# Optimization experiments

Measured on AMD Instinct MI355X. Metric: run time of the kernel, lower is better.

## Reference

```python
import math
import jax, jax.numpy as jnp
import numpy as np


def setup_inputs() -> dict:
    key = jax.random.key(0)
    k0, k1, k2 = jax.random.split(key, 3)
    b, c, h, w = 4, 256, 64, 64
    x = jax.random.normal(k0, (b, c, h, w), dtype=jnp.float32)
    # 1x1 conv weights stored as [out_ch, in_ch]
    qkv_w = jax.random.normal(k1, (3 * c, c), dtype=jnp.float32) / math.sqrt(c)
    qkv_b = jnp.zeros((3 * c,), dtype=jnp.float32)
    out_w = jax.random.normal(k2, (c, c), dtype=jnp.float32) / math.sqrt(c)
    out_b = jnp.zeros((c,), dtype=jnp.float32)
    return {"x": x, "qkv_w": qkv_w, "qkv_b": qkv_b, "out_w": out_w, "out_b": out_b}


def reference(x, qkv_w, qkv_b, out_w, out_b):
    b, c, h, w = x.shape
    n = h * w
    # 1x1 conv QKV projection: [b, 3c, h, w]
    qkv = jnp.einsum('oc,bchw->bohw', qkv_w, x) + qkv_b[None, :, None, None]
    # chunk along channels into q, k, v each [b, c, n]
    qkv = qkv.reshape(b, 3, c, n)
    q, k, v = qkv[:, 0], qkv[:, 1], qkv[:, 2]
    # attn[b, i, j] = sum_c k[b,c,i] * q[b,c,j] / sqrt(c); softmax over key axis (dim=-2 -> axis=1)
    scores = jnp.einsum('bcn,bcm->bnm', k, q) / math.sqrt(c)
    attn = jax.nn.softmax(scores, axis=1)
    # out[b, c, j] = sum_i v[b,c,i] * attn[b,i,j]
    o = jnp.einsum('bcn,bnm->bcm', v, attn).reshape(b, c, h, w)
    # output 1x1 conv
    return jnp.einsum('oc,bchw->bohw', out_w, o) + out_b[None, :, None, None]
```

## Files before the change

### kernel.cpp

```cpp
#include <hip/hip_runtime.h>
#include <hip/hip_bf16.h>

typedef unsigned short u16;
typedef unsigned int u32;
typedef __attribute__((ext_vector_type(8))) short short8;
typedef __attribute__((ext_vector_type(4))) short short4v;
typedef __attribute__((ext_vector_type(16))) float f32x16;

#define MFMA32 __builtin_amdgcn_mfma_f32_32x32x16_bf16

#define NSEQ 4096
#define CD 256
#define CF 0.09016844005556021f

__device__ __forceinline__ u16 f2bf(float f) {
  u32 u = __float_as_uint(f);
  u += 0x7fffu + ((u >> 16) & 1u);
  return (u16)(u >> 16);
}
__device__ __forceinline__ float bf2f(short s) {
  return __uint_as_float(((u32)(u16)s) << 16);
}
__device__ __forceinline__ u32 pk2bf(float a, float b) {
  union {
    __hip_bfloat162 h;
    u32 u;
  } cv;
  cv.h = __float22bfloat162_rn(make_float2(a, b));
  return cv.u;
}
__device__ __forceinline__ void async16(const void* g, void* l) {
  __builtin_amdgcn_global_load_lds(
      (const __attribute__((address_space(1))) u32*)g,
      (__attribute__((address_space(3))) u32*)l, 16, 0, 0);
}

__global__ void cast_w(const float* __restrict__ qkv_w,
                       const float* __restrict__ out_w, u16* __restrict__ wq,
                       u16* __restrict__ wo) {
  int idx = blockIdx.x * 256 + threadIdx.x;
  if (idx < 768 * CD) wq[idx] = f2bf(qkv_w[idx]);
  if (idx < CD * CD) wo[idx] = f2bf(out_w[idx]);
}

__global__ __launch_bounds__(256) void xpose(const float* __restrict__ x,
                                             u16* __restrict__ x_t) {
  __shared__ float tile[64][65];
  const int t = threadIdx.x;
  const int b = blockIdx.z;
  const int n0 = blockIdx.x * 64, c0 = blockIdx.y * 64;
  const float* xb = x + (size_t)b * CD * NSEQ;
  const int cr = t >> 4, nc4 = (t & 15) * 4;
#pragma unroll
  for (int i = 0; i < 4; ++i) {
    int c = cr + 16 * i;
    float4 v = *(const float4*)(xb + (size_t)(c0 + c) * NSEQ + n0 + nc4);
    tile[c][nc4 + 0] = v.x;
    tile[c][nc4 + 1] = v.y;
    tile[c][nc4 + 2] = v.z;
    tile[c][nc4 + 3] = v.w;
  }
  __syncthreads();
  const int n = t & 63, cc = (t >> 6) * 16;
  u16* dst = x_t + (size_t)b * NSEQ * CD + (size_t)(n0 + n) * CD + c0 + cc;
#pragma unroll
  for (int j = 0; j < 4; ++j) {
    short4v pv;
#pragma unroll
    for (int r = 0; r < 4; ++r) pv[r] = (short)f2bf(tile[cc + 4 * j + r][n]);
    *(short4v*)(dst + 4 * j) = pv;
  }
}

__global__ __launch_bounds__(512, 1) void qkv_gemm3(
    const u16* __restrict__ wq, const float* __restrict__ qkv_b,
    const u16* __restrict__ x_t, u16* __restrict__ q_t, u16* __restrict__ k_t,
    u16* __restrict__ v_) {
  __shared__ u16 __align__(16) Wls[128 * 256];
  __shared__ u16 __align__(16) Bls[128 * 256];
  const int t = threadIdx.x, w = t >> 6, lane = t & 63;
  const int l31 = lane & 31, l5 = lane >> 5;
  const int os = w & 3, nh = w >> 2;
  const int n0 = blockIdx.x * 128, o0 = blockIdx.y * 128, b = blockIdx.z;
  const u16* Xb = x_t + (size_t)b * NSEQ * CD;
#pragma unroll
  for (int j = 0; j < 8; ++j) {
    int r = w * 16 + j * 2 + l5;
    async16(wq + (size_t)(o0 + r) * CD + ((l31 ^ (r & 7)) * 8),
            Wls + (w * 16 + j * 2) * 256);
    async16(Xb + (size_t)(n0 + r) * CD + ((l31 ^ (r & 7)) * 8),
            Bls + (w * 16 + j * 2) * 256);
  }
  __builtin_amdgcn_s_waitcnt(0);
  __syncthreads();
  f32x16 acc0, acc1;
#pragma unroll
  for (int i = 0; i < 16; ++i) {
    acc0[i] = 0.f;
    acc1[i] = 0.f;
  }
  const int ra = os * 32 + l31;
  const int rb0 = nh * 64 + l31, rb1 = rb0 + 32;
#pragma unroll
  for (int kc = 0; kc < 16; ++kc) {
    short8 a = *(const short8*)(Wls + ra * 256 + (((kc * 2 + l5) ^ (ra & 7)) * 8));
    short8 b0 = *(const short8*)(Bls + rb0 * 256 + (((kc * 2 + l5) ^ (rb0 & 7)) * 8));
    short8 b1 = *(const short8*)(Bls + rb1 * 256 + (((kc * 2 + l5) ^ (rb1 & 7)) * 8));
    acc0 = MFMA32(a, b0, acc0, 0, 0, 0);
    acc1 = MFMA32(a, b1, acc1, 0, 0, 0);
  }
  const int otype = blockIdx.y >> 1;
  const int obase = o0 + os * 32;
#pragma unroll
  for (int na = 0; na < 2; ++na) {
    f32x16& acc = na ? acc1 : acc0;
    const int n_g = n0 + nh * 64 + na * 32 + l31;
    if (otype < 2) {
      u16* dst = (otype == 0 ? q_t : k_t) + (size_t)b * NSEQ * CD +
                 (size_t)n_g * CD + (obase - otype * 256);
#pragma unroll
      for (int g = 0; g < 4; ++g) {
        float4 bv = *(const float4*)(qkv_b + obase + g * 8 + l5 * 4);
        const float* bp = (const float*)&bv;
        short4v pk;
#pragma unroll
        for (int r = 0; r < 4; ++r) pk[r] = (short)f2bf(acc[g * 4 + r] + bp[r]);
        *(short4v*)(dst + g * 8 + l5 * 4) = pk;
      }
    } else {
      u16* dst = v_ + (size_t)b * CD * NSEQ;
#pragma unroll
      for (int g = 0; g < 4; ++g) {
        float4 bv = *(const float4*)(qkv_b + obase + g * 8 + l5 * 4);
        const float* bp = (const float*)&bv;
#pragma unroll
        for (int r = 0; r < 4; ++r) {
          int c = obase - 512 + g * 8 + l5 * 4 + r;
          dst[(size_t)c * NSEQ + n_g] = f2bf(acc[g * 4 + r] + bp[r]);
        }
      }
    }
  }
}

__global__ __launch_bounds__(512, 1) void flash6(const u16* __restrict__ q_t,
                                                 const u16* __restrict__ k_t,
                                                 const u16* __restrict__ v_,
                                                 u16* __restrict__ opart,
                                                 float2* __restrict__ ml) {
  __shared__ u16 __align__(16) Kls[2][64 * 256];
  __shared__ u16 __align__(16) Vls[2][256 * 64];

  const int t = threadIdx.x, w = t >> 6, lane = t & 63;
  const int l31 = lane & 31, l5 = lane >> 5;
  const int s = w >> 1, ch = (w & 1) * 128;

  const int linear = blockIdx.x;
  const int xcd = linear & 7, slot = linear >> 3;
  const int b = xcd >> 1, half = xcd & 1;
  const int m0 = slot * 128;
  const int nbase = half * 2048;

  const u16* Qb = q_t + (size_t)b * NSEQ * CD;
  const u16* Kb = k_t + (size_t)b * NSEQ * CD;
  const u16* Vb = v_ + (size_t)b * CD * NSEQ;

  const int lm = s * 32 + l31;
  const int mrow = m0 + lm;

  short8 qf[16];
#pragma unroll
  for (int kc = 0; kc < 16; ++kc)
    qf[kc] = *(const short8*)(Qb + (size_t)mrow * CD + kc * 16 + l5 * 8);

  const int kr = w * 8;
  const int vrb = w * 32;
  const int vr_lane = lane >> 3, vc_lane = lane & 7;

#pragma unroll
  for (int j = 0; j < 4; ++j) {
    int r = kr + j * 2 + l5;
    async16(Kb + (size_t)(nbase + r) * CD + ((l31 ^ (r & 7)) * 8),
            &Kls[0][(kr + j * 2) * 256]);
    int rv = vrb + j * 8 + vr_lane;
    async16(Vb + (size_t)rv * NSEQ + nbase + ((vc_lane ^ (rv & 7)) * 8),
            &Vls[0][(vrb + j * 8) * 64]);
  }

  float mst = -3.0e38f, lst = 0.f;
  f32x16 oa[4];
#pragma unroll
  for (int i = 0; i < 4; ++i)
#pragma unroll
    for (int r = 0; r < 16; ++r) oa[i][r] = 0.f;

  for (int tt = 0; tt < 32; ++tt) {
    const int cur = tt & 1;
    __builtin_amdgcn_s_waitcnt(0);
    __syncthreads();
    if (tt + 1 < 32) {
      const int n0 = nbase + (tt + 1) * 64;
      const int nxt = cur ^ 1;
#pragma unroll
      for (int j = 0; j < 4; ++j) {
        int r = kr + j * 2 + l5;
        async16(Kb + (size_t)(n0 + r) * CD + ((l31 ^ (r & 7)) * 8),
                &Kls[nxt][(kr + j * 2) * 256]);
        int rv = vrb + j * 8 + vr_lane;
        async16(Vb + (size_t)rv * NSEQ + n0 + ((vc_lane ^ (rv & 7)) * 8),
                &Vls[nxt][(vrb + j * 8) * 64]);
      }
    }
    f32x16 sa, sb;
#pragma unroll
    for (int i = 0; i < 16; ++i) {
      sa[i] = 0.f;
      sb[i] = 0.f;
    }
    const int rk0 = l31, rk1 = 32 + l31;
#pragma unroll
    for (int kc = 0; kc < 16; ++kc) {
      short8 a0 =
          *(const short8*)(&Kls[cur][rk0 * 256 + (((kc * 2 + l5) ^ (l31 & 7)) * 8)]);
      short8 a1 =
          *(const short8*)(&Kls[cur][rk1 * 256 + (((kc * 2 + l5) ^ (l31 & 7)) * 8)]);
      sa = MFMA32(a0, qf[kc], sa, 0, 0, 0);
      sb = MFMA32(a1, qf[kc], sb, 0, 0, 0);
    }
    float rm = sa[0];
#pragma unroll
    for (int i = 1; i < 16; ++i) rm = fmaxf(rm, sa[i]);
#pragma unroll
    for (int i = 0; i < 16; ++i) rm = fmaxf(rm, sb[i]);
    rm = fmaxf(rm, __shfl_xor(rm, 32));
    float mnew = fmaxf(mst, rm * CF);
    float al = exp2f(mst - mnew);
    mst = mnew;
    u32 d[2][4][2];
    float ls = 0.f;
#pragma unroll
    for (int a = 0; a < 2; ++a) {
      f32x16& sv = a ? sb : sa;
#pragma unroll
      for (int gg = 0; gg < 4; ++gg) {
        float p0 = exp2f(sv[gg * 4 + 0] * CF - mnew);
        float p1 = exp2f(sv[gg * 4 + 1] * CF - mnew);
        float p2 = exp2f(sv[gg * 4 + 2] * CF - mnew);
        float p3 = exp2f(sv[gg * 4 + 3] * CF - mnew);
        ls += (p0 + p1) + (p2 + p3);
        d[a][gg][0] = pk2bf(p0, p1);
        d[a][gg][1] = pk2bf(p2, p3);
      }
    }
    ls += __shfl_xor(ls, 32);
    lst = lst * al + ls;
    if (__ballot(al != 1.0f)) {
#pragma unroll
      for (int i = 0; i < 4; ++i)
#pragma unroll
        for (int r = 0; r < 16; ++r) oa[i][r] *= al;
    }
    short8 pf[4];
#pragma unroll
    for (int f = 0; f < 4; ++f) {
      const int a = f >> 1, g0 = (f & 1) * 2;
      u32 n0d = d[a][g0][0], n1d = d[a][g0][1];
      u32 m0d = d[a][g0 + 1][0], m1d = d[a][g0 + 1][1];
      u32 s0 = l5 ? n0d : m0d;
      u32 s1 = l5 ? n1d : m1d;
      u32 e0 = (u32)__shfl_xor((int)s0, 32);
      u32 e1 = (u32)__shfl_xor((int)s1, 32);
      union {
        u32 u[4];
        short8 s8;
      } cv;
      cv.u[0] = l5 ? e0 : n0d;
      cv.u[1] = l5 ? e1 : n1d;
      cv.u[2] = l5 ? m0d : e0;
      cv.u[3] = l5 ? m1d : e1;
      pf[f] = cv.s8;
    }
#pragma unroll
    for (int f = 0; f < 4; ++f) {
#pragma unroll
      for (int ct = 0; ct < 4; ++ct) {
        int c = ch + ct * 32 + l31;
        short8 vf =
            *(const short8*)(&Vls[cur][c * 64 + (((f * 2 + l5) ^ (c & 7)) * 8)]);
        oa[ct] = MFMA32(vf, pf[f], oa[ct], 0, 0, 0);
      }
    }
  }

  float inv = 1.0f / lst;
  u16* dst = opart + ((size_t)(half * 4 + b) * NSEQ + mrow) * CD;
#pragma unroll
  for (int ct = 0; ct < 4; ++ct)
#pragma unroll
    for (int gg = 0; gg < 4; ++gg) {
      short4v pk;
#pragma unroll
      for (int r = 0; r < 4; ++r) pk[r] = (short)f2bf(oa[ct][gg * 4 + r] * inv);
      *(short4v*)(dst + ch + ct * 32 + gg * 8 + l5 * 4) = pk;
    }
  if ((w & 1) == 0 && lane < 32)
    ml[(size_t)(half * 4 + b) * NSEQ + m0 + s * 32 + lane] =
        make_float2(mst, lst);
}

__global__ __launch_bounds__(512, 1) void out_gemm5(
    const u16* __restrict__ wo, const float* __restrict__ out_b,
    const u16* __restrict__ opart, const float2* __restrict__ ml,
    float* __restrict__ out) {
  __shared__ u16 __align__(16) Wls[128 * 256];
  __shared__ u16 __align__(16) Bls[128 * 256];
  const int t = threadIdx.x, w = t >> 6, lane = t & 63;
  const int l31 = lane & 31, l5 = lane >> 5;
  const int os = w & 3, nh = w >> 2;
  const int n0 = blockIdx.x * 128, o0 = blockIdx.y * 128, b = blockIdx.z;
#pragma unroll
  for (int j = 0; j < 8; ++j) {
    int r = w * 16 + j * 2 + l5;
    async16(wo + (size_t)(o0 + r) * CD + ((l31 ^ (r & 7)) * 8),
            Wls + (w * 16 + j * 2) * 256);
  }
  const u16* O1 = opart + (size_t)b * NSEQ * CD;
  const u16* O2 = opart + (size_t)(4 + b) * NSEQ * CD;
  const float2* ml1 = ml + (size_t)b * NSEQ;
  const float2* ml2 = ml + (size_t)(4 + b) * NSEQ;
#pragma unroll
  for (int i = 0; i < 8; ++i) {
    int idx = i * 512 + t;
    int r = idx >> 5, p = idx & 31;
    int n = n0 + r;
    float2 s1 = ml1[n], s2 = ml2[n];
    float M = fmaxf(s1.x, s2.x);
    float w1 = s1.y * exp2f(s1.x - M), w2 = s2.y * exp2f(s2.x - M);
    float inv = 1.0f / (w1 + w2);
    w1 *= inv;
    w2 *= inv;
    short8 x1 = *(const short8*)(O1 + (size_t)n * CD + p * 8);
    short8 x2 = *(const short8*)(O2 + (size_t)n * CD + p * 8);
    short8 om;
#pragma unroll
    for (int e = 0; e < 8; ++e)
      om[e] = (short)f2bf(w1 * bf2f(x1[e]) + w2 * bf2f(x2[e]));
    *(short8*)(Bls + r * 256 + ((p ^ (r & 7)) * 8)) = om;
  }
  __builtin_amdgcn_s_waitcnt(0);
  __syncthreads();
  f32x16 acc0, acc1;
#pragma unroll
  for (int i = 0; i < 16; ++i) {
    acc0[i] = 0.f;
    acc1[i] = 0.f;
  }
  const int ra = os * 32 + l31;
  const int rb0 = nh * 64 + l31, rb1 = rb0 + 32;
#pragma unroll
  for (int kc = 0; kc < 16; ++kc) {
    short8 a = *(const short8*)(Wls + ra * 256 + (((kc * 2 + l5) ^ (ra & 7)) * 8));
    short8 b0 = *(const short8*)(Bls + rb0 * 256 + (((kc * 2 + l5) ^ (rb0 & 7)) * 8));
    short8 b1 = *(const short8*)(Bls + rb1 * 256 + (((kc * 2 + l5) ^ (rb1 & 7)) * 8));
    acc0 = MFMA32(a, b0, acc0, 0, 0, 0);
    acc1 = MFMA32(a, b1, acc1, 0, 0, 0);
  }
  const int obase = o0 + os * 32;
#pragma unroll
  for (int na = 0; na < 2; ++na) {
    f32x16& acc = na ? acc1 : acc0;
    const int n_g = n0 + nh * 64 + na * 32 + l31;
#pragma unroll
    for (int g = 0; g < 4; ++g) {
      float4 bv = *(const float4*)(out_b + obase + g * 8 + l5 * 4);
      const float* bp = (const float*)&bv;
#pragma unroll
      for (int r = 0; r < 4; ++r) {
        int o = obase + g * 8 + l5 * 4 + r;
        out[((size_t)b * CD + o) * NSEQ + n_g] = acc[g * 4 + r] + bp[r];
      }
    }
  }
}

extern "C" void kernel_launch(void* const* d_in, const int* in_sizes, int n_in,
                              void* d_out, int out_size, void* d_ws,
                              size_t ws_size, hipStream_t stream) {
  const float* x = (const float*)d_in[0];
  const float* qkv_w = (const float*)d_in[1];
  const float* qkv_b = (const float*)d_in[2];
  const float* out_w = (const float*)d_in[3];
  const float* out_b = (const float*)d_in[4];
  float* out = (float*)d_out;

  const size_t SZ = (size_t)4 * NSEQ * CD;
  u16* x_t = (u16*)d_ws;
  u16* q_t = x_t + SZ;
  u16* k_t = q_t + SZ;
  u16* v_ = k_t + SZ;
  u16* opart = v_ + SZ;
  u16* wq = opart + 2 * SZ;
  u16* wo = wq + 768 * CD;
  float2* ml = (float2*)(wo + CD * CD);

  cast_w<<<dim3(768), dim3(256), 0, stream>>>(qkv_w, out_w, wq, wo);
  xpose<<<dim3(64, 4, 4), dim3(256), 0, stream>>>(x, x_t);
  qkv_gemm3<<<dim3(32, 6, 4), dim3(512), 0, stream>>>(wq, qkv_b, x_t, q_t, k_t,
                                                      v_);
  flash6<<<dim3(256), dim3(512), 0, stream>>>(q_t, k_t, v_, opart, ml);
  out_gemm5<<<dim3(32, 2, 4), dim3(512), 0, stream>>>(wo, out_b, opart, ml,
                                                      out);
}
```

Measured before the change: 231.2 us.

## Split KV tile across wave pairs and merge four partial outputs

In the flash kernel, each pair of waves now splits the 64-key tile in half by key instead of splitting the 256 output channels. Each wave computes a single 32x32 score block and accumulates all 256 channels for its key half. The result is four partial outputs per query (two sequence halves times two wave halves), and the output GEMM merges them with log-sum-exp weights. This halves the QK^T MFMA and softmax work per wave, which removes the duplicated score computation. In exchange it doubles the accumulator registers, doubles the partial-output memory traffic, and asks for 2 blocks per CU through launch_bounds even though the shared-memory footprint likely prevents that.

```diff
diff --git a/kernel.cpp b/kernel.cpp
--- a/kernel.cpp
+++ b/kernel.cpp
@@ -143,7 +143,7 @@
   }
 }
 
-__global__ __launch_bounds__(512, 1) void flash6(const u16* __restrict__ q_t,
+__global__ __launch_bounds__(512, 2) void flash7(const u16* __restrict__ q_t,
                                                  const u16* __restrict__ k_t,
                                                  const u16* __restrict__ v_,
                                                  u16* __restrict__ opart,
@@ -153,20 +153,20 @@
 
   const int t = threadIdx.x, w = t >> 6, lane = t & 63;
   const int l31 = lane & 31, l5 = lane >> 5;
-  const int s = w >> 1, ch = (w & 1) * 128;
+  const int s = w >> 1, nh = w & 1;
 
   const int linear = blockIdx.x;
   const int xcd = linear & 7, slot = linear >> 3;
   const int b = xcd >> 1, half = xcd & 1;
   const int m0 = slot * 128;
   const int nbase = half * 2048;
+  const int sid = half * 2 + nh;
 
   const u16* Qb = q_t + (size_t)b * NSEQ * CD;
   const u16* Kb = k_t + (size_t)b * NSEQ * CD;
   const u16* Vb = v_ + (size_t)b * CD * NSEQ;
 
-  const int lm = s * 32 + l31;
-  const int mrow = m0 + lm;
+  const int mrow = m0 + s * 32 + l31;
 
   short8 qf[16];
 #pragma unroll
@@ -188,9 +188,9 @@
   }
 
   float mst = -3.0e38f, lst = 0.f;
-  f32x16 oa[4];
-#pragma unroll
-  for (int i = 0; i < 4; ++i)
+  f32x16 oa[8];
+#pragma unroll
+  for (int i = 0; i < 8; ++i)
 #pragma unroll
     for (int r = 0; r < 16; ++r) oa[i][r] = 0.f;
 
@@ -211,104 +211,89 @@
                 &Vls[nxt][(vrb + j * 8) * 64]);
       }
     }
-    f32x16 sa, sb;
-#pragma unroll
-    for (int i = 0; i < 16; ++i) {
-      sa[i] = 0.f;
-      sb[i] = 0.f;
-    }
-    const int rk0 = l31, rk1 = 32 + l31;
+    f32x16 sa;
+#pragma unroll
+    for (int i = 0; i < 16; ++i) sa[i] = 0.f;
+    const int rk = nh * 32 + l31;
 #pragma unroll
     for (int kc = 0; kc < 16; ++kc) {
-      short8 a0 =
-          *(const short8*)(&Kls[cur][rk0 * 256 + (((kc * 2 + l5) ^ (l31 & 7)) * 8)]);
-      short8 a1 =
-          *(const short8*)(&Kls[cur][rk1 * 256 + (((kc * 2 + l5) ^ (l31 & 7)) * 8)]);
-      sa = MFMA32(a0, qf[kc], sa, 0, 0, 0);
-      sb = MFMA32(a1, qf[kc], sb, 0, 0, 0);
+      short8 a =
+          *(const short8*)(&Kls[cur][rk * 256 + (((kc * 2 + l5) ^ (rk & 7)) * 8)]);
+      sa = MFMA32(a, qf[kc], sa, 0, 0, 0);
     }
     float rm = sa[0];
 #pragma unroll
     for (int i = 1; i < 16; ++i) rm = fmaxf(rm, sa[i]);
-#pragma unroll
-    for (int i = 0; i < 16; ++i) rm = fmaxf(rm, sb[i]);
     rm = fmaxf(rm, __shfl_xor(rm, 32));
     float mnew = fmaxf(mst, rm * CF);
     float al = exp2f(mst - mnew);
     mst = mnew;
-    u32 d[2][4][2];
+    u32 d[4][2];
     float ls = 0.f;
 #pragma unroll
-    for (int a = 0; a < 2; ++a) {
-      f32x16& sv = a ? sb : sa;
-#pragma unroll
-      for (int gg = 0; gg < 4; ++gg) {
-        float p0 = exp2f(sv[gg * 4 + 0] * CF - mnew);
-        float p1 = exp2f(sv[gg * 4 + 1] * CF - mnew);
-        float p2 = exp2f(sv[gg * 4 + 2] * CF - mnew);
-        float p3 = exp2f(sv[gg * 4 + 3] * CF - mnew);
-        ls += (p0 + p1) + (p2 + p3);
-        d[a][gg][0] = pk2bf(p0, p1);
-        d[a][gg][1] = pk2bf(p2, p3);
-      }
+    for (int gg = 0; gg < 4; ++gg) {
+      float p0 = exp2f(sa[gg * 4 + 0] * CF - mnew);
+      float p1 = exp2f(sa[gg * 4 + 1] * CF - mnew);
+      float p2 = exp2f(sa[gg * 4 + 2] * CF - mnew);
+      float p3 = exp2f(sa[gg * 4 + 3] * CF - mnew);
+      ls += (p0 + p1) + (p2 + p3);
+      d[gg][0] = pk2bf(p0, p1);
+      d[gg][1] = pk2bf(p2, p3);
     }
     ls += __shfl_xor(ls, 32);
     lst = lst * al + ls;
     if (__ballot(al != 1.0f)) {
 #pragma unroll
-      for (int i = 0; i < 4; ++i)
+      for (int i = 0; i < 8; ++i)
 #pragma unroll
         for (int r = 0; r < 16; ++r) oa[i][r] *= al;
     }
-    short8 pf[4];
-#pragma unroll
-    for (int f = 0; f < 4; ++f) {
-      const int a = f >> 1, g0 = (f & 1) * 2;
-      u32 n0d = d[a][g0][0], n1d = d[a][g0][1];
-      u32 m0d = d[a][g0 + 1][0], m1d = d[a][g0 + 1][1];
-      u32 s0 = l5 ? n0d : m0d;
-      u32 s1 = l5 ? n1d : m1d;
-      u32 e0 = (u32)__shfl_xor((int)s0, 32);
-      u32 e1 = (u32)__shfl_xor((int)s1, 32);
+    short8 pf[2];
+#pragma unroll
+    for (int f = 0; f < 2; ++f) {
+      const int g0 = f * 2;
+      u32 sx0 = l5 ? d[g0][0] : d[g0 + 1][0];
+      u32 sx1 = l5 ? d[g0][1] : d[g0 + 1][1];
+      u32 e0 = (u32)__shfl_xor((int)sx0, 32);
+      u32 e1 = (u32)__shfl_xor((int)sx1, 32);
       union {
         u32 u[4];
         short8 s8;
       } cv;
-      cv.u[0] = l5 ? e0 : n0d;
-      cv.u[1] = l5 ? e1 : n1d;
-      cv.u[2] = l5 ? m0d : e0;
-      cv.u[3] = l5 ? m1d : e1;
+      cv.u[0] = l5 ? e0 : d[g0][0];
+      cv.u[1] = l5 ? e1 : d[g0][1];
+      cv.u[2] = l5 ? d[g0 + 1][0] : e0;
+      cv.u[3] = l5 ? d[g0 + 1][1] : e1;
       pf[f] = cv.s8;
     }
 #pragma unroll
-    for (int f = 0; f < 4; ++f) {
-#pragma unroll
-      for (int ct = 0; ct < 4; ++ct) {
-        int c = ch + ct * 32 + l31;
-        short8 vf =
-            *(const short8*)(&Vls[cur][c * 64 + (((f * 2 + l5) ^ (c & 7)) * 8)]);
+    for (int f = 0; f < 2; ++f) {
+#pragma unroll
+      for (int ct = 0; ct < 8; ++ct) {
+        int c = ct * 32 + l31;
+        short8 vf = *(const short8*)(&Vls[cur][c * 64 +
+                                               (((nh * 4 + f * 2 + l5) ^ (c & 7)) * 8)]);
         oa[ct] = MFMA32(vf, pf[f], oa[ct], 0, 0, 0);
       }
     }
   }
 
   float inv = 1.0f / lst;
-  u16* dst = opart + ((size_t)(half * 4 + b) * NSEQ + mrow) * CD;
-#pragma unroll
-  for (int ct = 0; ct < 4; ++ct)
+  u16* dst = opart + ((size_t)(sid * 4 + b) * NSEQ + mrow) * CD;
+#pragma unroll
+  for (int ct = 0; ct < 8; ++ct)
 #pragma unroll
     for (int gg = 0; gg < 4; ++gg) {
       short4v pk;
 #pragma unroll
       for (int r = 0; r < 4; ++r) pk[r] = (short)f2bf(oa[ct][gg * 4 + r] * inv);
-      *(short4v*)(dst + ch + ct * 32 + gg * 8 + l5 * 4) = pk;
-    }
-  if ((w & 1) == 0 && lane < 32)
-    ml[(size_t)(half * 4 + b) * NSEQ + m0 + s * 32 + lane] =
-        make_float2(mst, lst);
-}
-
-__global__ __launch_bounds__(512, 1) void out_gemm5(
+      *(short4v*)(dst + ct * 32 + gg * 8 + l5 * 4) = pk;
+    }
+  if (lane < 32)
+    ml[(size_t)(sid * 4 + b) * NSEQ + mrow] = make_float2(mst, lst);
+}
+
+__global__ __launch_bounds__(512, 1) void out_gemm6(
     const u16* __restrict__ wo, const float* __restrict__ out_b,
     const u16* __restrict__ opart, const float2* __restrict__ ml,
     float* __restrict__ out) {
@@ -324,27 +309,34 @@
     async16(wo + (size_t)(o0 + r) * CD + ((l31 ^ (r & 7)) * 8),
             Wls + (w * 16 + j * 2) * 256);
   }
-  const u16* O1 = opart + (size_t)b * NSEQ * CD;
-  const u16* O2 = opart + (size_t)(4 + b) * NSEQ * CD;
-  const float2* ml1 = ml + (size_t)b * NSEQ;
-  const float2* ml2 = ml + (size_t)(4 + b) * NSEQ;
 #pragma unroll
   for (int i = 0; i < 8; ++i) {
     int idx = i * 512 + t;
     int r = idx >> 5, p = idx & 31;
     int n = n0 + r;
-    float2 s1 = ml1[n], s2 = ml2[n];
-    float M = fmaxf(s1.x, s2.x);
-    float w1 = s1.y * exp2f(s1.x - M), w2 = s2.y * exp2f(s2.x - M);
-    float inv = 1.0f / (w1 + w2);
-    w1 *= inv;
-    w2 *= inv;
-    short8 x1 = *(const short8*)(O1 + (size_t)n * CD + p * 8);
-    short8 x2 = *(const short8*)(O2 + (size_t)n * CD + p * 8);
+    float2 st[4];
+#pragma unroll
+    for (int q = 0; q < 4; ++q) st[q] = ml[(size_t)(q * 4 + b) * NSEQ + n];
+    float M = fmaxf(fmaxf(st[0].x, st[1].x), fmaxf(st[2].x, st[3].x));
+    float wt[4], tot = 0.f;
+#pragma unroll
+    for (int q = 0; q < 4; ++q) {
+      wt[q] = st[q].y * exp2f(st[q].x - M);
+      tot += wt[q];
+    }
+    float inv = 1.0f / tot;
+    float acc[8] = {};
+#pragma unroll
+    for (int q = 0; q < 4; ++q) {
+      float wq_ = wt[q] * inv;
+      short8 xq =
+          *(const short8*)(opart + ((size_t)(q * 4 + b) * NSEQ + n) * CD + p * 8);
+#pragma unroll
+      for (int e = 0; e < 8; ++e) acc[e] += wq_ * bf2f(xq[e]);
+    }
     short8 om;
 #pragma unroll
-    for (int e = 0; e < 8; ++e)
-      om[e] = (short)f2bf(w1 * bf2f(x1[e]) + w2 * bf2f(x2[e]));
+    for (int e = 0; e < 8; ++e) om[e] = (short)f2bf(acc[e]);
     *(short8*)(Bls + r * 256 + ((p ^ (r & 7)) * 8)) = om;
   }
   __builtin_amdgcn_s_waitcnt(0);
@@ -399,7 +391,7 @@
   u16* k_t = q_t + SZ;
   u16* v_ = k_t + SZ;
   u16* opart = v_ + SZ;
-  u16* wq = opart + 2 * SZ;
+  u16* wq = opart + 4 * SZ;
   u16* wo = wq + 768 * CD;
   float2* ml = (float2*)(wo + CD * CD);
 
@@ -407,7 +399,7 @@
   xpose<<<dim3(64, 4, 4), dim3(256), 0, stream>>>(x, x_t);
   qkv_gemm3<<<dim3(32, 6, 4), dim3(512), 0, stream>>>(wq, qkv_b, x_t, q_t, k_t,
                                                       v_);
-  flash6<<<dim3(256), dim3(512), 0, stream>>>(q_t, k_t, v_, opart, ml);
-  out_gemm5<<<dim3(32, 2, 4), dim3(512), 0, stream>>>(wo, out_b, opart, ml,
+  flash7<<<dim3(256), dim3(512), 0, stream>>>(q_t, k_t, v_, opart, ml);
+  out_gemm6<<<dim3(32, 2, 4), dim3(512), 0, stream>>>(wo, out_b, opart, ml,
                                                       out);
 }
```

After: 230.3 us. No clear change (-0.4%).
